# Kernel optimization log

Measured on AMD Instinct MI355X. Metric: run time of the kernel, lower is better.

Reference implementation:

```python
import jax, jax.numpy as jnp
import numpy as np

N_EXPERTS = 8
D_MODEL = 1024
D_FFN = 4096
BATCH, SEQ = 4, 1024


def setup_inputs() -> dict:
    key = jax.random.key(0)
    ks = jax.random.split(key, 12)
    T = BATCH * SEQ
    s_d = 1.0 / np.sqrt(D_MODEL)
    s_f = 1.0 / np.sqrt(D_FFN)
    return {
        "x": jax.random.normal(ks[0], (BATCH, SEQ, D_MODEL), jnp.float32),
        "noise": jax.random.normal(ks[1], (T, N_EXPERTS), jnp.float32),
        # router (torch Linear stored as [out,in]; we store pre-transposed [in,out])
        "Wg": jax.random.uniform(ks[2], (D_MODEL, N_EXPERTS), jnp.float32, -s_d, s_d),
        "bg": jax.random.uniform(ks[3], (N_EXPERTS,), jnp.float32, -s_d, s_d),
        "Wn": jax.random.uniform(ks[4], (D_MODEL, N_EXPERTS), jnp.float32, -s_d, s_d),
        "bn": jax.random.uniform(ks[5], (N_EXPERTS,), jnp.float32, -s_d, s_d),
        # stacked expert weights: fc1 [E, D, F], fc2 [E, F, D]
        "W1": jax.random.uniform(ks[6], (N_EXPERTS, D_MODEL, D_FFN), jnp.float32, -s_d, s_d),
        "b1": jax.random.uniform(ks[7], (N_EXPERTS, D_FFN), jnp.float32, -s_d, s_d),
        "W2": jax.random.uniform(ks[8], (N_EXPERTS, D_FFN, D_MODEL), jnp.float32, -s_f, s_f),
        "b2": jax.random.uniform(ks[9], (N_EXPERTS, D_MODEL), jnp.float32, -s_f, s_f),
        "top_k": 2,
    }


def reference(x, noise, Wg, bg, Wn, bn, W1, b1, W2, b2, top_k):
    B, S, D = x.shape
    xf = x.reshape(-1, D)                       # [T, D]
    T = xf.shape[0]
    # --- noisy top-k router ---
    logits = xf @ Wg + bg                       # [T, E]
    noise_logits = xf @ Wn + bn                 # [T, E]
    noisy = logits + noise * jax.nn.softplus(noise_logits)
    top_v, top_i = jax.lax.top_k(noisy, top_k)  # [T, k]
    sparse = jnp.full_like(noisy, -jnp.inf)
    sparse = sparse.at[jnp.arange(T)[:, None], top_i].set(top_v)
    gates = jax.nn.softmax(sparse, axis=-1)     # [T, E], zeros off top-k
    # --- experts (dense grouped GEMM; non-selected tokens zeroed by gates) ---
    h = jax.nn.relu(jnp.einsum('td,edf->etf', xf, W1) + b1[:, None, :])  # [E, T, F]
    eo = jnp.einsum('etf,efd->etd', h, W2) + b2[:, None, :]              # [E, T, D]
    out = jnp.einsum('etd,te->td', eo, gates)                            # [T, D]
    return out.reshape(B, S, D)
```

## Files before the change

### kernel.cpp

```cpp
#include <hip/hip_runtime.h>
#include <math.h>

#define T_TOK 4096
#define DM 1024
#define DF 4096
#define NE 8

#define BM 128
#define BN 128
#define BK 32

typedef __attribute__((ext_vector_type(8))) short bf16x8;
typedef __attribute__((ext_vector_type(4))) float f32x4;
typedef unsigned long long u64;

__device__ __forceinline__ unsigned short f2bf(float f) {
    union { float f; unsigned int u; } v; v.f = f;
    unsigned int r = v.u + 0x7FFFu + ((v.u >> 16) & 1u);
    return (unsigned short)(r >> 16);
}
__device__ __forceinline__ float bf2f(unsigned short u) {
    union { float f; unsigned int u; } v; v.u = ((unsigned int)u) << 16;
    return v.f;
}

__device__ __forceinline__ void glds16(const void* g, void* l) {
    __builtin_amdgcn_global_load_lds(
        (const __attribute__((address_space(1))) unsigned int*)g,
        (__attribute__((address_space(3))) unsigned int*)l, 16, 0, 0);
}

__global__ __launch_bounds__(256) void k_router(
    const float* __restrict__ x, const float* __restrict__ noise,
    const float* __restrict__ Wg, const float* __restrict__ bg,
    const float* __restrict__ Wn, const float* __restrict__ bn,
    int* __restrict__ counts, int* __restrict__ slots, float* __restrict__ gates)
{
    const int lane = threadIdx.x & 63;
    const int wave = threadIdx.x >> 6;
    const int t = blockIdx.x * 4 + wave;
    const float* xr = x + (size_t)t * DM + lane * 16;

    float accg[8], accn[8];
    #pragma unroll
    for (int i = 0; i < 8; ++i) { accg[i] = 0.f; accn[i] = 0.f; }

    #pragma unroll
    for (int dd = 0; dd < 16; ++dd) {
        float xv = xr[dd];
        int d = lane * 16 + dd;
        float4 g0 = *(const float4*)(Wg + d * 8);
        float4 g1 = *(const float4*)(Wg + d * 8 + 4);
        float4 n0 = *(const float4*)(Wn + d * 8);
        float4 n1 = *(const float4*)(Wn + d * 8 + 4);
        accg[0] += xv * g0.x; accg[1] += xv * g0.y; accg[2] += xv * g0.z; accg[3] += xv * g0.w;
        accg[4] += xv * g1.x; accg[5] += xv * g1.y; accg[6] += xv * g1.z; accg[7] += xv * g1.w;
        accn[0] += xv * n0.x; accn[1] += xv * n0.y; accn[2] += xv * n0.z; accn[3] += xv * n0.w;
        accn[4] += xv * n1.x; accn[5] += xv * n1.y; accn[6] += xv * n1.z; accn[7] += xv * n1.w;
    }
    #pragma unroll
    for (int s = 1; s < 64; s <<= 1) {
        #pragma unroll
        for (int e = 0; e < 8; ++e) {
            accg[e] += __shfl_xor(accg[e], s, 64);
            accn[e] += __shfl_xor(accn[e], s, 64);
        }
    }
    if (lane == 0) {
        float nv[8];
        #pragma unroll
        for (int e = 0; e < 8; ++e) {
            float lg = accg[e] + bg[e];
            float nl = accn[e] + bn[e];
            float sp = (nl > 20.f) ? nl : log1pf(expf(nl));
            nv[e] = lg + noise[(size_t)t * NE + e] * sp;
        }
        int i0 = 0;
        #pragma unroll
        for (int e = 1; e < 8; ++e) if (nv[e] > nv[i0]) i0 = e;
        int i1 = -1;
        #pragma unroll
        for (int e = 0; e < 8; ++e) {
            if (e == i0) continue;
            if (i1 < 0 || nv[e] > nv[i1]) i1 = e;
        }
        float ex = expf(nv[i1] - nv[i0]);
        float g0 = 1.f / (1.f + ex);
        float g1 = ex / (1.f + ex);
        int p0 = atomicAdd(counts + i0, 1);
        slots[i0 * T_TOK + p0] = t * 2;     gates[i0 * T_TOK + p0] = g0;
        int p1 = atomicAdd(counts + i1, 1);
        slots[i1 * T_TOK + p1] = t * 2 + 1; gates[i1 * T_TOK + p1] = g1;
    }
}

__global__ __launch_bounds__(256) void k_xcast(const float* __restrict__ x,
                                               unsigned short* __restrict__ xb)
{
    int i = blockIdx.x * 256 + threadIdx.x;
    float4 v = ((const float4*)x)[i];
    u64 p = (u64)f2bf(v.x) | ((u64)f2bf(v.y) << 16) | ((u64)f2bf(v.z) << 32) | ((u64)f2bf(v.w) << 48);
    ((u64*)xb)[i] = p;
}

__global__ __launch_bounds__(256) void k_tr(const float* __restrict__ in,
                                            unsigned short* __restrict__ out,
                                            int R, int C)
{
    __shared__ unsigned short t[64 * 68];
    const int e = blockIdx.z;
    const int C0 = blockIdx.x * 64, R0 = blockIdx.y * 64;
    const float* ip = in + ((size_t)e * R + R0) * C + C0;
    unsigned short* op = out + ((size_t)e * C + C0) * R + R0;
    const int tid = threadIdx.x;

    #pragma unroll
    for (int p = 0; p < 4; ++p) {
        int r = p * 16 + (tid >> 4), c4 = (tid & 15) * 4;
        float4 v = *(const float4*)(ip + (size_t)r * C + c4);
        t[(c4 + 0) * 68 + r] = f2bf(v.x);
        t[(c4 + 1) * 68 + r] = f2bf(v.y);
        t[(c4 + 2) * 68 + r] = f2bf(v.z);
        t[(c4 + 3) * 68 + r] = f2bf(v.w);
    }
    __syncthreads();
    #pragma unroll
    for (int p = 0; p < 4; ++p) {
        int c = p * 16 + (tid >> 4), r4 = (tid & 15) * 4;
        u64 v = *(const u64*)(t + c * 68 + r4);
        *(u64*)(op + (size_t)c * R + r4) = v;
    }
}

__global__ __launch_bounds__(256, 4) void k_fc1(
    const unsigned short* __restrict__ xb, const unsigned short* __restrict__ W1t,
    const float* __restrict__ b1, const int* __restrict__ counts,
    const int* __restrict__ slots, unsigned short* __restrict__ h)
{
    const int e = blockIdx.x;
    const int cnt = counts[e];
    const int mt = blockIdx.z;
    if (mt * BM >= cnt) return;
    const int nb = blockIdx.y * BN;

    __shared__ unsigned short As[2][BM * BK];
    __shared__ unsigned short Bs[2][BN * BK];
    __shared__ int slot_s[BM];

    const int tid = threadIdx.x;
    if (tid < BM) {
        int gi = mt * BM + tid;
        slot_s[tid] = (gi < cnt) ? slots[e * T_TOK + gi] : -1;
    }
    __syncthreads();

    const int srow = tid >> 2;
    const int cg = (tid & 3) ^ ((tid >> 3) & 3);

    const unsigned short* ag[2];
    const unsigned short* bgp[2];
    const unsigned short* wbase = W1t + (size_t)e * DF * DM;
    #pragma unroll
    for (int c = 0; c < 2; ++c) {
        int row = c * 64 + srow;
        int s = slot_s[row];
        int tok = (s >= 0) ? (s >> 1) : 0;
        ag[c]  = xb + (size_t)tok * DM + cg * 8;
        bgp[c] = wbase + (size_t)(nb + row) * DM + cg * 8;
    }

    const int lane = tid & 63, wv = tid >> 6;
    const int wm = (wv & 1) * 64, wn = (wv >> 1) * 64;
    const int ml = lane & 15, kg = lane >> 4;
    const int rch = (kg ^ ((ml >> 1) & 3)) * 8;
    const int lo = wv * 512;

    f32x4 acc[4][4];
    #pragma unroll
    for (int ni = 0; ni < 4; ++ni)
        #pragma unroll
        for (int mi = 0; mi < 4; ++mi) acc[ni][mi] = (f32x4){0.f, 0.f, 0.f, 0.f};

    #pragma unroll
    for (int c = 0; c < 2; ++c) glds16(ag[c],  &As[0][c * 2048 + lo]);
    #pragma unroll
    for (int c = 0; c < 2; ++c) glds16(bgp[c], &Bs[0][c * 2048 + lo]);

    int buf = 0;
    for (int k0 = 0; k0 < DM; k0 += BK) {
        __syncthreads();
        if (k0 + BK < DM) {
            #pragma unroll
            for (int c = 0; c < 2; ++c) glds16(ag[c] + k0 + BK,  &As[buf ^ 1][c * 2048 + lo]);
            #pragma unroll
            for (int c = 0; c < 2; ++c) glds16(bgp[c] + k0 + BK, &Bs[buf ^ 1][c * 2048 + lo]);
        }
        bf16x8 af[4], bfr[4];
        #pragma unroll
        for (int mi = 0; mi < 4; ++mi)
            af[mi] = *(const bf16x8*)(&As[buf][(wm + mi * 16 + ml) * BK + rch]);
        #pragma unroll
        for (int ni = 0; ni < 4; ++ni)
            bfr[ni] = *(const bf16x8*)(&Bs[buf][(wn + ni * 16 + ml) * BK + rch]);
        #pragma unroll
        for (int ni = 0; ni < 4; ++ni)
            #pragma unroll
            for (int mi = 0; mi < 4; ++mi)
                acc[ni][mi] = __builtin_amdgcn_mfma_f32_16x16x32_bf16(bfr[ni], af[mi], acc[ni][mi], 0, 0, 0);
        buf ^= 1;
    }

    #pragma unroll
    for (int mi = 0; mi < 4; ++mi) {
        int s = slot_s[wm + mi * 16 + ml];
        if (s < 0) continue;
        #pragma unroll
        for (int ni = 0; ni < 4; ++ni) {
            int n0 = wn + ni * 16 + kg * 4;
            float4 bb = *(const float4*)(b1 + (size_t)e * DF + nb + n0);
            float v0 = fmaxf(acc[ni][mi][0] + bb.x, 0.f);
            float v1 = fmaxf(acc[ni][mi][1] + bb.y, 0.f);
            float v2 = fmaxf(acc[ni][mi][2] + bb.z, 0.f);
            float v3 = fmaxf(acc[ni][mi][3] + bb.w, 0.f);
            u64 p = (u64)f2bf(v0) | ((u64)f2bf(v1) << 16) | ((u64)f2bf(v2) << 32) | ((u64)f2bf(v3) << 48);
            *(u64*)(h + (size_t)s * DF + nb + n0) = p;
        }
    }
}

__global__ __launch_bounds__(256, 4) void k_fc2(
    const unsigned short* __restrict__ h, const unsigned short* __restrict__ W2t,
    const float* __restrict__ b2, const int* __restrict__ counts,
    const int* __restrict__ slots, const float* __restrict__ gates,
    unsigned short* __restrict__ eo)
{
    const int e = blockIdx.x;
    const int cnt = counts[e];
    const int mt = blockIdx.z >> 1;
    const int kz = blockIdx.z & 1;
    if (mt * BM >= cnt) return;
    const int nb = blockIdx.y * BN;

    __shared__ unsigned short As[2][BM * BK];
    __shared__ unsigned short Bs[2][BN * BK];
    __shared__ int slot_s[BM];
    __shared__ float gate_s[BM];

    const int tid = threadIdx.x;
    if (tid < BM) {
        int gi = mt * BM + tid;
        if (gi < cnt) {
            slot_s[tid] = slots[e * T_TOK + gi];
            gate_s[tid] = gates[e * T_TOK + gi];
        } else { slot_s[tid] = -1; gate_s[tid] = 0.f; }
    }
    __syncthreads();

    const int srow = tid >> 2;
    const int cg = (tid & 3) ^ ((tid >> 3) & 3);
    const int kbeg = kz * (DF / 2);

    const unsigned short* ag[2];
    const unsigned short* bgp[2];
    const unsigned short* wbase = W2t + (size_t)e * DM * DF;
    #pragma unroll
    for (int c = 0; c < 2; ++c) {
        int row = c * 64 + srow;
        int s = slot_s[row];
        int sl = (s >= 0) ? s : 0;
        ag[c]  = h + (size_t)sl * DF + kbeg + cg * 8;
        bgp[c] = wbase + (size_t)(nb + row) * DF + kbeg + cg * 8;
    }

    const int lane = tid & 63, wv = tid >> 6;
    const int wm = (wv & 1) * 64, wn = (wv >> 1) * 64;
    const int ml = lane & 15, kg = lane >> 4;
    const int rch = (kg ^ ((ml >> 1) & 3)) * 8;
    const int lo = wv * 512;

    f32x4 acc[4][4];
    #pragma unroll
    for (int ni = 0; ni < 4; ++ni)
        #pragma unroll
        for (int mi = 0; mi < 4; ++mi) acc[ni][mi] = (f32x4){0.f, 0.f, 0.f, 0.f};

    #pragma unroll
    for (int c = 0; c < 2; ++c) glds16(ag[c],  &As[0][c * 2048 + lo]);
    #pragma unroll
    for (int c = 0; c < 2; ++c) glds16(bgp[c], &Bs[0][c * 2048 + lo]);

    int buf = 0;
    for (int k0 = 0; k0 < DF / 2; k0 += BK) {
        __syncthreads();
        if (k0 + BK < DF / 2) {
            #pragma unroll
            for (int c = 0; c < 2; ++c) glds16(ag[c] + k0 + BK,  &As[buf ^ 1][c * 2048 + lo]);
            #pragma unroll
            for (int c = 0; c < 2; ++c) glds16(bgp[c] + k0 + BK, &Bs[buf ^ 1][c * 2048 + lo]);
        }
        bf16x8 af[4], bfr[4];
        #pragma unroll
        for (int mi = 0; mi < 4; ++mi)
            af[mi] = *(const bf16x8*)(&As[buf][(wm + mi * 16 + ml) * BK + rch]);
        #pragma unroll
        for (int ni = 0; ni < 4; ++ni)
            bfr[ni] = *(const bf16x8*)(&Bs[buf][(wn + ni * 16 + ml) * BK + rch]);
        #pragma unroll
        for (int ni = 0; ni < 4; ++ni)
            #pragma unroll
            for (int mi = 0; mi < 4; ++mi)
                acc[ni][mi] = __builtin_amdgcn_mfma_f32_16x16x32_bf16(bfr[ni], af[mi], acc[ni][mi], 0, 0, 0);
        buf ^= 1;
    }

    unsigned short* eob = eo + (size_t)kz * 2 * T_TOK * DM;
    #pragma unroll
    for (int mi = 0; mi < 4; ++mi) {
        int s = slot_s[wm + mi * 16 + ml];
        if (s < 0) continue;
        float g = gate_s[wm + mi * 16 + ml];
        #pragma unroll
        for (int ni = 0; ni < 4; ++ni) {
            int n0 = wn + ni * 16 + kg * 4;
            float4 bb;
            if (kz == 0) bb = *(const float4*)(b2 + (size_t)e * DM + nb + n0);
            else         bb = make_float4(0.f, 0.f, 0.f, 0.f);
            float v0 = g * (acc[ni][mi][0] + bb.x);
            float v1 = g * (acc[ni][mi][1] + bb.y);
            float v2 = g * (acc[ni][mi][2] + bb.z);
            float v3 = g * (acc[ni][mi][3] + bb.w);
            u64 p = (u64)f2bf(v0) | ((u64)f2bf(v1) << 16) | ((u64)f2bf(v2) << 32) | ((u64)f2bf(v3) << 48);
            *(u64*)(eob + (size_t)s * DM + nb + n0) = p;
        }
    }
}

__global__ __launch_bounds__(256) void k_comb(const unsigned short* __restrict__ eo,
                                              float* __restrict__ out)
{
    int i = blockIdx.x * 256 + threadIdx.x;
    int t = i >> 8;
    int d4 = (i & 255) * 4;
    const unsigned short* p0 = eo + (size_t)(2 * t) * DM + d4;
    const unsigned short* p1 = p0 + DM;
    const unsigned short* q0 = p0 + (size_t)2 * T_TOK * DM;
    const unsigned short* q1 = q0 + DM;
    ushort4 a0 = *(const ushort4*)p0;
    ushort4 a1 = *(const ushort4*)p1;
    ushort4 b0 = *(const ushort4*)q0;
    ushort4 b1 = *(const ushort4*)q1;
    float4 r;
    r.x = bf2f(a0.x) + bf2f(a1.x) + bf2f(b0.x) + bf2f(b1.x);
    r.y = bf2f(a0.y) + bf2f(a1.y) + bf2f(b0.y) + bf2f(b1.y);
    r.z = bf2f(a0.z) + bf2f(a1.z) + bf2f(b0.z) + bf2f(b1.z);
    r.w = bf2f(a0.w) + bf2f(a1.w) + bf2f(b0.w) + bf2f(b1.w);
    ((float4*)out)[i] = r;
}

extern "C" void kernel_launch(void* const* d_in, const int* in_sizes, int n_in,
                              void* d_out, int out_size, void* d_ws, size_t ws_size,
                              hipStream_t stream) {
    const float* x     = (const float*)d_in[0];
    const float* noise = (const float*)d_in[1];
    const float* Wg    = (const float*)d_in[2];
    const float* bg    = (const float*)d_in[3];
    const float* Wn    = (const float*)d_in[4];
    const float* bn    = (const float*)d_in[5];
    const float* W1    = (const float*)d_in[6];
    const float* b1    = (const float*)d_in[7];
    const float* W2    = (const float*)d_in[8];
    const float* b2    = (const float*)d_in[9];
    float* out = (float*)d_out;

    char* ws = (char*)d_ws;
    int*   counts = (int*)ws;
    int*   slots  = (int*)(ws + 4096);
    float* gates  = (float*)(ws + 4096 + NE * T_TOK * 4);
    unsigned short* xb = (unsigned short*)(ws + 4096 + 2 * NE * T_TOK * 4);
    unsigned short* hh = xb + (size_t)T_TOK * DM;
    unsigned short* Wt = hh + (size_t)2 * T_TOK * DF;
    unsigned short* eo = Wt + (size_t)NE * DM * DF;

    hipMemsetAsync(counts, 0, 4096, stream);

    k_router<<<T_TOK / 4, 256, 0, stream>>>(x, noise, Wg, bg, Wn, bn, counts, slots, gates);
    k_xcast<<<T_TOK * DM / 1024, 256, 0, stream>>>(x, xb);

    k_tr<<<dim3(DF / 64, DM / 64, NE), 256, 0, stream>>>(W1, Wt, DM, DF);
    k_fc1<<<dim3(NE, DF / BN, T_TOK / BM), 256, 0, stream>>>(xb, Wt, b1, counts, slots, hh);

    k_tr<<<dim3(DM / 64, DF / 64, NE), 256, 0, stream>>>(W2, Wt, DF, DM);
    k_fc2<<<dim3(NE, DM / BN, (T_TOK / BM) * 2), 256, 0, stream>>>(hh, Wt, b2, counts, slots, gates, eo);

    k_comb<<<T_TOK * DM / 1024, 256, 0, stream>>>(eo, out);
}
```

Before: 670.1 us.

## Fuse x cast into router, widen BK, single-buffer LDS, compact h rows

After: 760.3 us. 1.13x slower.

```diff
diff --git a/kernel.cpp b/kernel.cpp
--- a/kernel.cpp
+++ b/kernel.cpp
@@ -8,7 +8,7 @@
 
 #define BM 128
 #define BN 128
-#define BK 32
+#define BK 64
 
 typedef __attribute__((ext_vector_type(8))) short bf16x8;
 typedef __attribute__((ext_vector_type(4))) float f32x4;
@@ -23,6 +23,9 @@
     union { float f; unsigned int u; } v; v.u = ((unsigned int)u) << 16;
     return v.f;
 }
+__device__ __forceinline__ u64 pk4(float4 a) {
+    return (u64)f2bf(a.x) | ((u64)f2bf(a.y) << 16) | ((u64)f2bf(a.z) << 32) | ((u64)f2bf(a.w) << 48);
+}
 
 __device__ __forceinline__ void glds16(const void* g, void* l) {
     __builtin_amdgcn_global_load_lds(
@@ -34,29 +37,41 @@
     const float* __restrict__ x, const float* __restrict__ noise,
     const float* __restrict__ Wg, const float* __restrict__ bg,
     const float* __restrict__ Wn, const float* __restrict__ bn,
-    int* __restrict__ counts, int* __restrict__ slots, float* __restrict__ gates)
+    int* __restrict__ counts, int* __restrict__ slots, float* __restrict__ gates,
+    unsigned short* __restrict__ xb)
 {
     const int lane = threadIdx.x & 63;
     const int wave = threadIdx.x >> 6;
     const int t = blockIdx.x * 4 + wave;
-    const float* xr = x + (size_t)t * DM + lane * 16;
+    const float* xr = x + (size_t)t * DM;
+
+    float4 xv[4];
+    #pragma unroll
+    for (int j = 0; j < 4; ++j) xv[j] = *(const float4*)(xr + j * 256 + lane * 4);
+    #pragma unroll
+    for (int j = 0; j < 4; ++j)
+        *(u64*)(xb + (size_t)t * DM + j * 256 + lane * 4) = pk4(xv[j]);
 
     float accg[8], accn[8];
     #pragma unroll
     for (int i = 0; i < 8; ++i) { accg[i] = 0.f; accn[i] = 0.f; }
 
     #pragma unroll
-    for (int dd = 0; dd < 16; ++dd) {
-        float xv = xr[dd];
-        int d = lane * 16 + dd;
-        float4 g0 = *(const float4*)(Wg + d * 8);
-        float4 g1 = *(const float4*)(Wg + d * 8 + 4);
-        float4 n0 = *(const float4*)(Wn + d * 8);
-        float4 n1 = *(const float4*)(Wn + d * 8 + 4);
-        accg[0] += xv * g0.x; accg[1] += xv * g0.y; accg[2] += xv * g0.z; accg[3] += xv * g0.w;
-        accg[4] += xv * g1.x; accg[5] += xv * g1.y; accg[6] += xv * g1.z; accg[7] += xv * g1.w;
-        accn[0] += xv * n0.x; accn[1] += xv * n0.y; accn[2] += xv * n0.z; accn[3] += xv * n0.w;
-        accn[4] += xv * n1.x; accn[5] += xv * n1.y; accn[6] += xv * n1.z; accn[7] += xv * n1.w;
+    for (int j = 0; j < 4; ++j) {
+        const float xs[4] = {xv[j].x, xv[j].y, xv[j].z, xv[j].w};
+        #pragma unroll
+        for (int jj = 0; jj < 4; ++jj) {
+            int d = j * 256 + lane * 4 + jj;
+            float xvv = xs[jj];
+            float4 g0 = *(const float4*)(Wg + d * 8);
+            float4 g1 = *(const float4*)(Wg + d * 8 + 4);
+            float4 n0 = *(const float4*)(Wn + d * 8);
+            float4 n1 = *(const float4*)(Wn + d * 8 + 4);
+            accg[0] += xvv * g0.x; accg[1] += xvv * g0.y; accg[2] += xvv * g0.z; accg[3] += xvv * g0.w;
+            accg[4] += xvv * g1.x; accg[5] += xvv * g1.y; accg[6] += xvv * g1.z; accg[7] += xvv * g1.w;
+            accn[0] += xvv * n0.x; accn[1] += xvv * n0.y; accn[2] += xvv * n0.z; accn[3] += xvv * n0.w;
+            accn[4] += xvv * n1.x; accn[5] += xvv * n1.y; accn[6] += xvv * n1.z; accn[7] += xvv * n1.w;
+        }
     }
     #pragma unroll
     for (int s = 1; s < 64; s <<= 1) {
@@ -92,15 +107,6 @@
         int p1 = atomicAdd(counts + i1, 1);
         slots[i1 * T_TOK + p1] = t * 2 + 1; gates[i1 * T_TOK + p1] = g1;
     }
-}
-
-__global__ __launch_bounds__(256) void k_xcast(const float* __restrict__ x,
-                                               unsigned short* __restrict__ xb)
-{
-    int i = blockIdx.x * 256 + threadIdx.x;
-    float4 v = ((const float4*)x)[i];
-    u64 p = (u64)f2bf(v.x) | ((u64)f2bf(v.y) << 16) | ((u64)f2bf(v.z) << 32) | ((u64)f2bf(v.w) << 48);
-    ((u64*)xb)[i] = p;
 }
 
 __global__ __launch_bounds__(256) void k_tr(const float* __restrict__ in,
@@ -143,8 +149,11 @@
     if (mt * BM >= cnt) return;
     const int nb = blockIdx.y * BN;
 
-    __shared__ unsigned short As[2][BM * BK];
-    __shared__ unsigned short Bs[2][BN * BK];
+    int offE = 0;
+    for (int i = 0; i < e; ++i) offE += counts[i];
+
+    __shared__ unsigned short As[BM * BK];
+    __shared__ unsigned short Bs[BN * BK];
     __shared__ int slot_s[BM];
 
     const int tid = threadIdx.x;
@@ -154,26 +163,26 @@
     }
     __syncthreads();
 
-    const int srow = tid >> 2;
-    const int cg = (tid & 3) ^ ((tid >> 3) & 3);
-
-    const unsigned short* ag[2];
-    const unsigned short* bgp[2];
+    const int lane = tid & 63, wv = tid >> 6;
+    const int srow = tid >> 3;
+    const int g = (tid & 7) ^ (srow & 7);
+
+    const unsigned short* agp[4];
+    const unsigned short* bgp[4];
     const unsigned short* wbase = W1t + (size_t)e * DF * DM;
     #pragma unroll
-    for (int c = 0; c < 2; ++c) {
-        int row = c * 64 + srow;
+    for (int cc = 0; cc < 4; ++cc) {
+        int row = cc * 32 + srow;
         int s = slot_s[row];
         int tok = (s >= 0) ? (s >> 1) : 0;
-        ag[c]  = xb + (size_t)tok * DM + cg * 8;
-        bgp[c] = wbase + (size_t)(nb + row) * DM + cg * 8;
-    }
-
-    const int lane = tid & 63, wv = tid >> 6;
+        agp[cc] = xb + (size_t)tok * DM + g * 8;
+        bgp[cc] = wbase + (size_t)(nb + row) * DM + g * 8;
+    }
+    unsigned short* al = As + wv * 512;
+    unsigned short* bl = Bs + wv * 512;
+
     const int wm = (wv & 1) * 64, wn = (wv >> 1) * 64;
     const int ml = lane & 15, kg = lane >> 4;
-    const int rch = (kg ^ ((ml >> 1) & 3)) * 8;
-    const int lo = wv * 512;
 
     f32x4 acc[4][4];
     #pragma unroll
@@ -181,39 +190,37 @@
         #pragma unroll
         for (int mi = 0; mi < 4; ++mi) acc[ni][mi] = (f32x4){0.f, 0.f, 0.f, 0.f};
 
-    #pragma unroll
-    for (int c = 0; c < 2; ++c) glds16(ag[c],  &As[0][c * 2048 + lo]);
-    #pragma unroll
-    for (int c = 0; c < 2; ++c) glds16(bgp[c], &Bs[0][c * 2048 + lo]);
-
-    int buf = 0;
     for (int k0 = 0; k0 < DM; k0 += BK) {
+        #pragma unroll
+        for (int cc = 0; cc < 4; ++cc) glds16(agp[cc] + k0, al + cc * 2048);
+        #pragma unroll
+        for (int cc = 0; cc < 4; ++cc) glds16(bgp[cc] + k0, bl + cc * 2048);
         __syncthreads();
-        if (k0 + BK < DM) {
-            #pragma unroll
-            for (int c = 0; c < 2; ++c) glds16(ag[c] + k0 + BK,  &As[buf ^ 1][c * 2048 + lo]);
-            #pragma unroll
-            for (int c = 0; c < 2; ++c) glds16(bgp[c] + k0 + BK, &Bs[buf ^ 1][c * 2048 + lo]);
-        }
-        bf16x8 af[4], bfr[4];
-        #pragma unroll
-        for (int mi = 0; mi < 4; ++mi)
-            af[mi] = *(const bf16x8*)(&As[buf][(wm + mi * 16 + ml) * BK + rch]);
-        #pragma unroll
-        for (int ni = 0; ni < 4; ++ni)
-            bfr[ni] = *(const bf16x8*)(&Bs[buf][(wn + ni * 16 + ml) * BK + rch]);
-        #pragma unroll
-        for (int ni = 0; ni < 4; ++ni)
+        #pragma unroll
+        for (int ks = 0; ks < 2; ++ks) {
+            const int rch = (((ks * 4 + kg) ^ (ml & 7)) << 3);
+            bf16x8 af[4], bfr[4];
             #pragma unroll
             for (int mi = 0; mi < 4; ++mi)
-                acc[ni][mi] = __builtin_amdgcn_mfma_f32_16x16x32_bf16(bfr[ni], af[mi], acc[ni][mi], 0, 0, 0);
-        buf ^= 1;
+                af[mi] = *(const bf16x8*)(As + (wm + mi * 16 + ml) * BK + rch);
+            #pragma unroll
+            for (int ni = 0; ni < 4; ++ni)
+                bfr[ni] = *(const bf16x8*)(Bs + (wn + ni * 16 + ml) * BK + rch);
+            #pragma unroll
+            for (int ni = 0; ni < 4; ++ni)
+                #pragma unroll
+                for (int mi = 0; mi < 4; ++mi)
+                    acc[ni][mi] = __builtin_amdgcn_mfma_f32_16x16x32_bf16(bfr[ni], af[mi], acc[ni][mi], 0, 0, 0);
+        }
+        __syncthreads();
     }
 
     #pragma unroll
     for (int mi = 0; mi < 4; ++mi) {
-        int s = slot_s[wm + mi * 16 + ml];
+        int row = wm + mi * 16 + ml;
+        int s = slot_s[row];
         if (s < 0) continue;
+        unsigned short* hrow = h + (size_t)(offE + mt * BM + row) * DF + nb;
         #pragma unroll
         for (int ni = 0; ni < 4; ++ni) {
             int n0 = wn + ni * 16 + kg * 4;
@@ -223,7 +230,7 @@
             float v2 = fmaxf(acc[ni][mi][2] + bb.z, 0.f);
             float v3 = fmaxf(acc[ni][mi][3] + bb.w, 0.f);
             u64 p = (u64)f2bf(v0) | ((u64)f2bf(v1) << 16) | ((u64)f2bf(v2) << 32) | ((u64)f2bf(v3) << 48);
-            *(u64*)(h + (size_t)s * DF + nb + n0) = p;
+            *(u64*)(hrow + n0) = p;
         }
     }
 }
@@ -241,8 +248,11 @@
     if (mt * BM >= cnt) return;
     const int nb = blockIdx.y * BN;
 
-    __shared__ unsigned short As[2][BM * BK];
-    __shared__ unsigned short Bs[2][BN * BK];
+    int offE = 0;
+    for (int i = 0; i < e; ++i) offE += counts[i];
+
+    __shared__ unsigned short As[BM * BK];
+    __shared__ unsigned short Bs[BN * BK];
     __shared__ int slot_s[BM];
     __shared__ float gate_s[BM];
 
@@ -256,27 +266,27 @@
     }
     __syncthreads();
 
-    const int srow = tid >> 2;
-    const int cg = (tid & 3) ^ ((tid >> 3) & 3);
+    const int lane = tid & 63, wv = tid >> 6;
+    const int srow = tid >> 3;
+    const int g = (tid & 7) ^ (srow & 7);
     const int kbeg = kz * (DF / 2);
 
-    const unsigned short* ag[2];
-    const unsigned short* bgp[2];
+    const unsigned short* agp[4];
+    const unsigned short* bgp[4];
     const unsigned short* wbase = W2t + (size_t)e * DM * DF;
     #pragma unroll
-    for (int c = 0; c < 2; ++c) {
-        int row = c * 64 + srow;
-        int s = slot_s[row];
-        int sl = (s >= 0) ? s : 0;
-        ag[c]  = h + (size_t)sl * DF + kbeg + cg * 8;
-        bgp[c] = wbase + (size_t)(nb + row) * DF + kbeg + cg * 8;
-    }
-
-    const int lane = tid & 63, wv = tid >> 6;
+    for (int cc = 0; cc < 4; ++cc) {
+        int row = cc * 32 + srow;
+        int gi = mt * BM + row;
+        int gpos = offE + ((gi < cnt) ? gi : 0);
+        agp[cc] = h + (size_t)gpos * DF + kbeg + g * 8;
+        bgp[cc] = wbase + (size_t)(nb + row) * DF + kbeg + g * 8;
+    }
+    unsigned short* al = As + wv * 512;
+    unsigned short* bl = Bs + wv * 512;
+
     const int wm = (wv & 1) * 64, wn = (wv >> 1) * 64;
     const int ml = lane & 15, kg = lane >> 4;
-    const int rch = (kg ^ ((ml >> 1) & 3)) * 8;
-    const int lo = wv * 512;
 
     f32x4 acc[4][4];
     #pragma unroll
@@ -284,51 +294,48 @@
         #pragma unroll
         for (int mi = 0; mi < 4; ++mi) acc[ni][mi] = (f32x4){0.f, 0.f, 0.f, 0.f};
 
-    #pragma unroll
-    for (int c = 0; c < 2; ++c) glds16(ag[c],  &As[0][c * 2048 + lo]);
-    #pragma unroll
-    for (int c = 0; c < 2; ++c) glds16(bgp[c], &Bs[0][c * 2048 + lo]);
-
-    int buf = 0;
     for (int k0 = 0; k0 < DF / 2; k0 += BK) {
+        #pragma unroll
+        for (int cc = 0; cc < 4; ++cc) glds16(agp[cc] + k0, al + cc * 2048);
+        #pragma unroll
+        for (int cc = 0; cc < 4; ++cc) glds16(bgp[cc] + k0, bl + cc * 2048);
         __syncthreads();
-        if (k0 + BK < DF / 2) {
-            #pragma unroll
-            for (int c = 0; c < 2; ++c) glds16(ag[c] + k0 + BK,  &As[buf ^ 1][c * 2048 + lo]);
-            #pragma unroll
-            for (int c = 0; c < 2; ++c) glds16(bgp[c] + k0 + BK, &Bs[buf ^ 1][c * 2048 + lo]);
-        }
-        bf16x8 af[4], bfr[4];
-        #pragma unroll
-        for (int mi = 0; mi < 4; ++mi)
-            af[mi] = *(const bf16x8*)(&As[buf][(wm + mi * 16 + ml) * BK + rch]);
-        #pragma unroll
-        for (int ni = 0; ni < 4; ++ni)
-            bfr[ni] = *(const bf16x8*)(&Bs[buf][(wn + ni * 16 + ml) * BK + rch]);
-        #pragma unroll
-        for (int ni = 0; ni < 4; ++ni)
+        #pragma unroll
+        for (int ks = 0; ks < 2; ++ks) {
+            const int rch = (((ks * 4 + kg) ^ (ml & 7)) << 3);
+            bf16x8 af[4], bfr[4];
             #pragma unroll
             for (int mi = 0; mi < 4; ++mi)
-                acc[ni][mi] = __builtin_amdgcn_mfma_f32_16x16x32_bf16(bfr[ni], af[mi], acc[ni][mi], 0, 0, 0);
-        buf ^= 1;
+                af[mi] = *(const bf16x8*)(As + (wm + mi * 16 + ml) * BK + rch);
+            #pragma unroll
+            for (int ni = 0; ni < 4; ++ni)
+                bfr[ni] = *(const bf16x8*)(Bs + (wn + ni * 16 + ml) * BK + rch);
+            #pragma unroll
+            for (int ni = 0; ni < 4; ++ni)
+                #pragma unroll
+                for (int mi = 0; mi < 4; ++mi)
+                    acc[ni][mi] = __builtin_amdgcn_mfma_f32_16x16x32_bf16(bfr[ni], af[mi], acc[ni][mi], 0, 0, 0);
+        }
+        __syncthreads();
     }
 
     unsigned short* eob = eo + (size_t)kz * 2 * T_TOK * DM;
     #pragma unroll
     for (int mi = 0; mi < 4; ++mi) {
-        int s = slot_s[wm + mi * 16 + ml];
+        int row = wm + mi * 16 + ml;
+        int s = slot_s[row];
         if (s < 0) continue;
-        float g = gate_s[wm + mi * 16 + ml];
+        float gg = gate_s[row];
         #pragma unroll
         for (int ni = 0; ni < 4; ++ni) {
             int n0 = wn + ni * 16 + kg * 4;
             float4 bb;
             if (kz == 0) bb = *(const float4*)(b2 + (size_t)e * DM + nb + n0);
             else         bb = make_float4(0.f, 0.f, 0.f, 0.f);
-            float v0 = g * (acc[ni][mi][0] + bb.x);
-            float v1 = g * (acc[ni][mi][1] + bb.y);
-            float v2 = g * (acc[ni][mi][2] + bb.z);
-            float v3 = g * (acc[ni][mi][3] + bb.w);
+            float v0 = gg * (acc[ni][mi][0] + bb.x);
+            float v1 = gg * (acc[ni][mi][1] + bb.y);
+            float v2 = gg * (acc[ni][mi][2] + bb.z);
+            float v3 = gg * (acc[ni][mi][3] + bb.w);
             u64 p = (u64)f2bf(v0) | ((u64)f2bf(v1) << 16) | ((u64)f2bf(v2) << 32) | ((u64)f2bf(v3) << 48);
             *(u64*)(eob + (size_t)s * DM + nb + n0) = p;
         }
@@ -383,8 +390,7 @@
 
     hipMemsetAsync(counts, 0, 4096, stream);
 
-    k_router<<<T_TOK / 4, 256, 0, stream>>>(x, noise, Wg, bg, Wn, bn, counts, slots, gates);
-    k_xcast<<<T_TOK * DM / 1024, 256, 0, stream>>>(x, xb);
+    k_router<<<T_TOK / 4, 256, 0, stream>>>(x, noise, Wg, bg, Wn, bn, counts, slots, gates, xb);
 
     k_tr<<<dim3(DF / 64, DM / 64, NE), 256, 0, stream>>>(W1, Wt, DM, DF);
     k_fc1<<<dim3(NE, DF / BN, T_TOK / BM), 256, 0, stream>>>(xb, Wt, b1, counts, slots, hh);
```
